# Kernel tuning notes

Hardware: AMD Instinct MI355X
Metric: run time of the kernel (lower is better)

Reference implementation:

```python
import jax, jax.numpy as jnp
import numpy as np

B, C, D, H, W = 1, 128, 8, 32, 32
NH, HD = 8, 16            # num_heads, head_dim = C // NH
PD, PH, PW = 2, 4, 4      # local patch dims
RD, RH, RW = 2, 2, 2      # global K/V reduction ratios
MLPH = 4 * C              # mlp_ratio = 4
EPS = 1e-5
SCALE = HD ** -0.5


def setup_inputs() -> dict:
    key = jax.random.key(0)
    ks = iter(jax.random.split(key, 16))
    def w(shape, scale=0.02):
        return jax.random.normal(next(ks), shape, jnp.float32) * scale
    inp = {"x": jax.random.normal(next(ks), (B, C, D, H, W), jnp.float32)}
    for p in ("l", "g"):  # local branch / global branch transformer blocks
        inp[f"{p}_n1_g"] = jnp.ones((C,), jnp.float32)
        inp[f"{p}_n1_b"] = jnp.zeros((C,), jnp.float32)
        inp[f"{p}_qkv_w"] = w((3 * C, C))            # Linear(dim, 3*dim, bias=False)
        inp[f"{p}_proj_w"] = w((C, C))
        inp[f"{p}_proj_b"] = jnp.zeros((C,), jnp.float32)
        inp[f"{p}_n2_g"] = jnp.ones((C,), jnp.float32)
        inp[f"{p}_n2_b"] = jnp.zeros((C,), jnp.float32)
        inp[f"{p}_fc1_w"] = w((MLPH, C))
        inp[f"{p}_fc1_b"] = jnp.zeros((MLPH,), jnp.float32)
        inp[f"{p}_fc2_w"] = w((C, MLPH))
        inp[f"{p}_fc2_b"] = jnp.zeros((C,), jnp.float32)
    inp["g_ke_w"] = w((C, C, RD, RH, RW))  # Conv3d(dim, dim, k=stride=(2,2,2), bias=False)
    inp["g_ve_w"] = w((C, C, RD, RH, RW))
    inp["g_nk_g"] = jnp.ones((HD,), jnp.float32)
    inp["g_nk_b"] = jnp.zeros((HD,), jnp.float32)
    inp["g_nv_g"] = jnp.ones((HD,), jnp.float32)
    inp["g_nv_b"] = jnp.zeros((HD,), jnp.float32)
    return inp


def _ln(t, g, b):
    m = t.mean(-1, keepdims=True)
    v = jnp.square(t - m).mean(-1, keepdims=True)
    return (t - m) * jax.lax.rsqrt(v + EPS) * g + b


def _mlp(t, w1, b1, w2, b2):
    return jax.nn.gelu(t @ w1.T + b1, approximate=False) @ w2.T + b2


def _forward(x, l_n1_g, l_n1_b, l_qkv_w, l_proj_w, l_proj_b, l_n2_g, l_n2_b,
             l_fc1_w, l_fc1_b, l_fc2_w, l_fc2_b,
             g_n1_g, g_n1_b, g_qkv_w, g_ke_w, g_ve_w, g_nk_g, g_nk_b,
             g_nv_g, g_nv_b, g_proj_w, g_proj_b, g_n2_g, g_n2_b,
             g_fc1_w, g_fc1_b, g_fc2_w, g_fc2_b):
    nd, nh, nw = D // PD, H // PH, W // PW
    R, Npl = nd * nh * nw, PD * PH * PW
    N = D * H * W

    # ---------------- Local branch ----------------
    # (B,C,D,H,W) -> (B, R, Npl, C) patch tokens
    loc = x.reshape(B, C, nd, PD, nh, PH, nw, PW)
    loc = loc.transpose(0, 2, 4, 6, 3, 5, 7, 1).reshape(B, R, Npl, C)
    y = _ln(loc, l_n1_g, l_n1_b)
    qkv = (y @ l_qkv_w.T).reshape(B, R, Npl, 3, NH, HD).transpose(3, 0, 1, 4, 2, 5)
    q, k, v = qkv[0], qkv[1], qkv[2]  # (B,R,NH,Npl,HD)
    attn = jax.nn.softmax(jnp.einsum('brhnd,brhmd->brhnm', q, k) * SCALE, axis=-1)
    o = jnp.einsum('brhnm,brhmd->brhnd', attn, v)
    # faithful to torch: (attn@v).transpose(-1,-2).reshape(B,R,Npl,C)
    o = jnp.swapaxes(o, -1, -2).reshape(B, R, Npl, C)
    loc = loc + (o @ l_proj_w.T + l_proj_b)
    loc = loc + _mlp(_ln(loc, l_n2_g, l_n2_b), l_fc1_w, l_fc1_b, l_fc2_w, l_fc2_b)
    # back to (B,C,D,H,W)
    loc_y = loc.reshape(B, nd, nh, nw, PD, PH, PW, C)
    loc_y = loc_y.transpose(0, 7, 1, 4, 2, 5, 3, 6).reshape(B, C, D, H, W)

    # ---------------- Global branch ----------------
    g = x.reshape(B, C, N).transpose(0, 2, 1)  # (B,N,C)
    y = _ln(g, g_n1_g, g_n1_b)
    qkv = y @ g_qkv_w.T  # (B,N,3C)
    q, k, v = jnp.split(qkv, 3, axis=-1)
    qh = q.reshape(B, N, NH, HD).transpose(0, 2, 1, 3)  # (B,NH,N,HD)
    dn = ('NCDHW', 'OIDHW', 'NCDHW')
    def _reduce(t, wc):
        tm = t.transpose(0, 2, 1).reshape(B, C, D, H, W)
        tr = jax.lax.conv_general_dilated(tm, wc, (RD, RH, RW), 'VALID',
                                          dimension_numbers=dn)
        nr = tr.shape[2] * tr.shape[3] * tr.shape[4]
        return tr.reshape(B, C, nr).transpose(0, 2, 1).reshape(B, nr, NH, HD).transpose(0, 2, 1, 3)
    kr = _ln(_reduce(k, g_ke_w), g_nk_g, g_nk_b)  # (B,NH,Nr,HD)
    vr = _ln(_reduce(v, g_ve_w), g_nv_g, g_nv_b)
    attn = jax.nn.softmax(jnp.einsum('bhnd,bhmd->bhnm', qh, kr) * SCALE, axis=-1)
    o = jnp.einsum('bhnm,bhmd->bhnd', attn, vr)
    o = o.transpose(0, 2, 1, 3).reshape(B, N, C)
    g = g + (o @ g_proj_w.T + g_proj_b)
    g = g + _mlp(_ln(g, g_n2_g, g_n2_b), g_fc1_w, g_fc1_b, g_fc2_w, g_fc2_b)
    glo_y = g.transpose(0, 2, 1).reshape(B, C, D, H, W)

    # ---------------- Gate ----------------
    return x * jax.nn.sigmoid(loc_y + glo_y)


def reference(x, l_n1_g, l_n1_b, l_qkv_w, l_proj_w, l_proj_b, l_n2_g, l_n2_b,
              l_fc1_w, l_fc1_b, l_fc2_w, l_fc2_b,
              g_n1_g, g_n1_b, g_qkv_w, g_ke_w, g_ve_w, g_nk_g, g_nk_b,
              g_nv_g, g_nv_b, g_proj_w, g_proj_b, g_n2_g, g_n2_b,
              g_fc1_w, g_fc1_b, g_fc2_w, g_fc2_b):
    return _forward(x, l_n1_g, l_n1_b, l_qkv_w, l_proj_w, l_proj_b, l_n2_g, l_n2_b,
                    l_fc1_w, l_fc1_b, l_fc2_w, l_fc2_b,
                    g_n1_g, g_n1_b, g_qkv_w, g_ke_w, g_ve_w, g_nk_g, g_nk_b,
                    g_nv_g, g_nv_b, g_proj_w, g_proj_b, g_n2_g, g_n2_b,
                    g_fc1_w, g_fc1_b, g_fc2_w, g_fc2_b)
```

## Files before the change

### kernel.cpp

```cpp
#include <hip/hip_runtime.h>
#include <math.h>

#define N_TOK 8192
#define C_DIM 128
#define NHD   8
#define HDIM  16
#define NR    1024
#define EPSV  1e-5f
#define QK_SCALE 0.25f
#define QK_L2E  0.36067376f

typedef __attribute__((ext_vector_type(8))) short short8;
typedef __attribute__((ext_vector_type(4))) float f32x4;

__device__ __forceinline__ float gelu_f(float v) {
    float u = 0.7978845608f * (v + 0.044715f * v * v * v);
    float e = exp2f(2.885390082f * u);
    return v * (e / (e + 1.0f));
}
__device__ __forceinline__ float uaf(unsigned int u) {
    union { unsigned int u; float f; } x; x.u = u; return x.f;
}
__device__ __forceinline__ short f2b(float v) {
    union { float f; unsigned int u; } x; x.f = v;
    unsigned int r = x.u + 0x7fffu + ((x.u >> 16) & 1u);
    return (short)(r >> 16);
}
__device__ __forceinline__ unsigned int pk2(float a, float b) {
    return (unsigned int)(unsigned short)f2b(a) | ((unsigned int)(unsigned short)f2b(b) << 16);
}
__device__ __forceinline__ void ld16bf(const short* p, float* d) {
    uint4 a = *(const uint4*)p;
    uint4 b = *(const uint4*)(p + 8);
    d[0]  = uaf(a.x << 16); d[1]  = uaf(a.x & 0xffff0000u);
    d[2]  = uaf(a.y << 16); d[3]  = uaf(a.y & 0xffff0000u);
    d[4]  = uaf(a.z << 16); d[5]  = uaf(a.z & 0xffff0000u);
    d[6]  = uaf(a.w << 16); d[7]  = uaf(a.w & 0xffff0000u);
    d[8]  = uaf(b.x << 16); d[9]  = uaf(b.x & 0xffff0000u);
    d[10] = uaf(b.y << 16); d[11] = uaf(b.y & 0xffff0000u);
    d[12] = uaf(b.z << 16); d[13] = uaf(b.z & 0xffff0000u);
    d[14] = uaf(b.w << 16); d[15] = uaf(b.w & 0xffff0000u);
}

__device__ __forceinline__ void gload16(const void* g, void* l) {
    __builtin_amdgcn_global_load_lds(
        (const __attribute__((address_space(1))) unsigned int*)g,
        (__attribute__((address_space(3))) unsigned int*)l, 16, 0, 0);
}

struct CvtDesc { const float* src; short* dst; int n; int pad; };
struct CvtArgs { CvtDesc d[10]; };

__global__ __launch_bounds__(256) void prep_k(const float* __restrict__ x,
                                              const float* __restrict__ g1, const float* __restrict__ b1,
                                              const float* __restrict__ g2, const float* __restrict__ b2,
                                              float* __restrict__ xt,
                                              short* __restrict__ o1, short* __restrict__ o2,
                                              CvtArgs ca) {
    __shared__ float tile[32][132];
    int t = threadIdx.x;
    if (blockIdx.x >= 256) {
        int bid = blockIdx.x - 256;
#pragma unroll 1
        for (int d = 0; d < 10; ++d) {
            CvtDesc dd = ca.d[d];
            if (dd.pad) {
                for (int i = bid * 256 + t; i < dd.n; i += 40 * 256) {
                    int co = i >> 10, qq = i & 1023;
                    dd.dst[co * 1024 + ((qq & 7) << 7) + (qq >> 3)] = f2b(dd.src[i]);
                }
            } else {
                for (int i = bid * 256 + t; i < dd.n; i += 40 * 256)
                    dd.dst[i] = f2b(dd.src[i]);
            }
        }
        return;
    }
    int n0 = blockIdx.x * 32;
#pragma unroll
    for (int k = 0; k < 16; ++k) {
        int f = t + k * 256;
        int n = f & 31, c = f >> 5;
        tile[n][c] = x[(size_t)c * N_TOK + n0 + n];
    }
    __syncthreads();
    int tk = t >> 3, cb = (t & 7) * 16;
    float v[16];
    float s = 0.f, sq = 0.f;
#pragma unroll
    for (int i = 0; i < 16; ++i) {
        v[i] = tile[tk][cb + i];
        s += v[i]; sq += v[i] * v[i];
    }
    s += __shfl_xor(s, 1);  s += __shfl_xor(s, 2);  s += __shfl_xor(s, 4);
    sq += __shfl_xor(sq, 1); sq += __shfl_xor(sq, 2); sq += __shfl_xor(sq, 4);
    float m = s * (1.0f / 128.0f);
    float var = sq * (1.0f / 128.0f) - m * m;
    float rs = rsqrtf(var + EPSV);
    int tok = n0 + tk;
    float* xp = xt + (size_t)tok * C_DIM + cb;
    *(float4*)(xp)      = make_float4(v[0], v[1], v[2], v[3]);
    *(float4*)(xp + 4)  = make_float4(v[4], v[5], v[6], v[7]);
    *(float4*)(xp + 8)  = make_float4(v[8], v[9], v[10], v[11]);
    *(float4*)(xp + 12) = make_float4(v[12], v[13], v[14], v[15]);
    float hA[16], hB[16];
#pragma unroll
    for (int i = 0; i < 16; ++i) {
        float hn = (v[i] - m) * rs;
        hA[i] = hn * g1[cb + i] + b1[cb + i];
        hB[i] = hn * g2[cb + i] + b2[cb + i];
    }
    uint4 ua0 = {pk2(hA[0], hA[1]), pk2(hA[2], hA[3]), pk2(hA[4], hA[5]), pk2(hA[6], hA[7])};
    uint4 ua1 = {pk2(hA[8], hA[9]), pk2(hA[10], hA[11]), pk2(hA[12], hA[13]), pk2(hA[14], hA[15])};
    uint4 ub0 = {pk2(hB[0], hB[1]), pk2(hB[2], hB[3]), pk2(hB[4], hB[5]), pk2(hB[6], hB[7])};
    uint4 ub1 = {pk2(hB[8], hB[9]), pk2(hB[10], hB[11]), pk2(hB[12], hB[13]), pk2(hB[14], hB[15])};
    *(uint4*)(o1 + (size_t)tok * C_DIM + cb)     = ua0;
    *(uint4*)(o1 + (size_t)tok * C_DIM + cb + 8) = ua1;
    *(uint4*)(o2 + (size_t)tok * C_DIM + cb)     = ub0;
    *(uint4*)(o2 + (size_t)tok * C_DIM + cb + 8) = ub1;
}

__global__ __launch_bounds__(256) void ln2_pair_k(const float* __restrict__ in0,
                                                  const float* __restrict__ g0, const float* __restrict__ b0,
                                                  short* __restrict__ o0,
                                                  const float* __restrict__ in1,
                                                  const float* __restrict__ g1, const float* __restrict__ b1,
                                                  short* __restrict__ o1) {
    int blk = blockIdx.x;
    bool sel = blk >= 2048;
    blk &= 2047;
    const float* in = sel ? in1 : in0;
    const float* g  = sel ? g1 : g0;
    const float* b  = sel ? b1 : b0;
    short* o        = sel ? o1 : o0;
    int lane = threadIdx.x & 63;
    int n = blk * 4 + (threadIdx.x >> 6);
    float v0 = in[(size_t)n * C_DIM + lane];
    float v1 = in[(size_t)n * C_DIM + 64 + lane];
    float s = v0 + v1, sq = v0 * v0 + v1 * v1;
#pragma unroll
    for (int off = 32; off >= 1; off >>= 1) {
        s += __shfl_xor(s, off);
        sq += __shfl_xor(sq, off);
    }
    float m = s * (1.0f / 128.0f);
    float var = sq * (1.0f / 128.0f) - m * m;
    float rs = rsqrtf(var + EPSV);
    o[(size_t)n * C_DIM + lane]      = f2b((v0 - m) * rs * g[lane] + b[lane]);
    o[(size_t)n * C_DIM + 64 + lane] = f2b((v1 - m) * rs * g[lane + 64] + b[lane + 64]);
}

struct MArgs {
    const short* A[2]; const short* W[2];
    const float* bias[2]; const float* res[2];
    void* out[2];
};
template <int EPI>
__global__ __launch_bounds__(256) void mgemm_k(MArgs ga, int M, int N, int K) {
    int zi = blockIdx.z;
    const short* A = ga.A[zi];
    const short* W = ga.W[zi];
    __shared__ short As[2][128 * 64];
    __shared__ short Bs[2][128 * 64];
    int t = threadIdx.x;
    int w = t >> 6, l = t & 63;
    int m0 = blockIdx.x * 128, n0 = blockIdx.y * 128;
    int wm = (w >> 1) * 64, wn = (w & 1) * 64;

    f32x4 acc[4][4];
#pragma unroll
    for (int a = 0; a < 4; ++a)
#pragma unroll
        for (int b = 0; b < 4; ++b) acc[a][b] = f32x4{0.f, 0.f, 0.f, 0.f};

    auto STAGE = [&](int buf, int k0) {
#pragma unroll
        for (int c = 0; c < 4; ++c) {
            int g0 = c * 256 + w * 64;
            int g  = g0 + l;
            int row = g >> 3, ss = g & 7;
            int slot = ss ^ (row & 7);
            gload16(A + (size_t)(m0 + row) * K + k0 + slot * 8, &As[buf][g0 * 8]);
            gload16(W + (size_t)(n0 + row) * K + k0 + slot * 8, &Bs[buf][g0 * 8]);
        }
    };

    int NT = K >> 6;
    STAGE(0, 0);
    int cur = 0;
    for (int it = 0; it < NT; ++it) {
        if (it + 1 < NT) {
            STAGE(cur ^ 1, (it + 1) << 6);
            asm volatile("s_waitcnt vmcnt(8)" ::: "memory");
        } else {
            asm volatile("s_waitcnt vmcnt(0)" ::: "memory");
        }
        __builtin_amdgcn_s_barrier();
#pragma unroll
        for (int kk = 0; kk < 2; ++kk) {
            short8 af[4], bf[4];
            int sl = kk * 4 + (l >> 4);
#pragma unroll
            for (int mf = 0; mf < 4; ++mf) {
                int row = wm + mf * 16 + (l & 15);
                af[mf] = *(const short8*)(&As[cur][row * 64 + (sl ^ (row & 7)) * 8]);
            }
#pragma unroll
            for (int nf = 0; nf < 4; ++nf) {
                int row = wn + nf * 16 + (l & 15);
                bf[nf] = *(const short8*)(&Bs[cur][row * 64 + (sl ^ (row & 7)) * 8]);
            }
#pragma unroll
            for (int mf = 0; mf < 4; ++mf)
#pragma unroll
                for (int nf = 0; nf < 4; ++nf)
                    acc[mf][nf] = __builtin_amdgcn_mfma_f32_16x16x32_bf16(
                        af[mf], bf[nf], acc[mf][nf], 0, 0, 0);
        }
        asm volatile("s_waitcnt lgkmcnt(0)" ::: "memory");
        __builtin_amdgcn_sched_barrier(0);
        __builtin_amdgcn_s_barrier();
        cur ^= 1;
    }

#pragma unroll
    for (int mf = 0; mf < 4; ++mf) {
#pragma unroll
        for (int nf = 0; nf < 4; ++nf) {
            int col = n0 + wn + nf * 16 + (l & 15);
#pragma unroll
            for (int j = 0; j < 4; ++j) {
                int row = m0 + wm + mf * 16 + (l >> 4) * 4 + j;
                float v = acc[mf][nf][j];
                if (EPI == 0) {
                    ((short*)ga.out[zi])[(size_t)row * N + col] = f2b(v);
                } else if (EPI == 1) {
                    v += ga.bias[zi][col] + ga.res[zi][(size_t)row * N + col];
                    ((float*)ga.out[zi])[(size_t)row * N + col] = v;
                } else if (EPI == 2) {
                    v = gelu_f(v + ga.bias[zi][col]);
                    ((short*)ga.out[zi])[(size_t)row * N + col] = f2b(v);
                }
            }
        }
    }
}

struct CLArgs {
    const short* qkv_g; const short* wk; const short* wv;
    float* kpart; float* vpart;
    const short* qkv_l; short* ob;
};
__global__ __launch_bounds__(256) void convlat_k(CLArgs ga) {
    __shared__ char smem[65536];
    int t = threadIdx.x;
    if (blockIdx.x < 128) {
        int bid = blockIdx.x;
        int m0 = (bid & 7) * 128;
        int zi = bid >> 6;
        int slice = (bid >> 3) & 7;
        const short* Abase = ga.qkv_g + (zi ? 256 : 128);
        const short* W = zi ? ga.wv : ga.wk;
        float* outp = zi ? ga.vpart : ga.kpart;
        short (*As)[8192] = (short(*)[8192])smem;
        short (*Bs)[8192] = (short(*)[8192])(smem + 32768);
        int w = t >> 6, l = t & 63;
        int wm = (w >> 1) * 64, wn = (w & 1) * 64;
        int kbeg = slice * 128;
        int od = slice >> 2, oh = (slice >> 1) & 1, ow = slice & 1;

        f32x4 acc[4][4];
#pragma unroll
        for (int a = 0; a < 4; ++a)
#pragma unroll
            for (int b = 0; b < 4; ++b) acc[a][b] = f32x4{0.f, 0.f, 0.f, 0.f};

        auto STAGE = [&](int buf, int k0) {
#pragma unroll
            for (int c = 0; c < 4; ++c) {
                int g0 = c * 256 + w * 64;
                int g  = g0 + l;
                int row = g >> 3, ss = g & 7;
                int slot = ss ^ (row & 7);
                int nr = m0 + row;
                int n = (2 * (nr >> 8) + od) * 1024 + (2 * ((nr >> 4) & 15) + oh) * 32
                        + 2 * (nr & 15) + ow;
                gload16(Abase + (size_t)n * 384 + (k0 & 127) + slot * 8, &As[buf][g0 * 8]);
                gload16(W + (size_t)row * 1024 + k0 + slot * 8, &Bs[buf][g0 * 8]);
            }
        };

        STAGE(0, kbeg);
        int cur = 0;
        for (int it = 0; it < 2; ++it) {
            if (it == 0) {
                STAGE(1, kbeg + 64);
                asm volatile("s_waitcnt vmcnt(8)" ::: "memory");
            } else {
                asm volatile("s_waitcnt vmcnt(0)" ::: "memory");
            }
            __builtin_amdgcn_s_barrier();
#pragma unroll
            for (int kk = 0; kk < 2; ++kk) {
                short8 af[4], bf[4];
                int sl = kk * 4 + (l >> 4);
#pragma unroll
                for (int mf = 0; mf < 4; ++mf) {
                    int row = wm + mf * 16 + (l & 15);
                    af[mf] = *(const short8*)(&As[cur][row * 64 + (sl ^ (row & 7)) * 8]);
                }
#pragma unroll
                for (int nf = 0; nf < 4; ++nf) {
                    int row = wn + nf * 16 + (l & 15);
                    bf[nf] = *(const short8*)(&Bs[cur][row * 64 + (sl ^ (row & 7)) * 8]);
                }
#pragma unroll
                for (int mf = 0; mf < 4; ++mf)
#pragma unroll
                    for (int nf = 0; nf < 4; ++nf)
                        acc[mf][nf] = __builtin_amdgcn_mfma_f32_16x16x32_bf16(
                            af[mf], bf[nf], acc[mf][nf], 0, 0, 0);
            }
            asm volatile("s_waitcnt lgkmcnt(0)" ::: "memory");
            __builtin_amdgcn_sched_barrier(0);
            __builtin_amdgcn_s_barrier();
            cur ^= 1;
        }
#pragma unroll
        for (int mf = 0; mf < 4; ++mf)
#pragma unroll
            for (int nf = 0; nf < 4; ++nf) {
                int col = wn + nf * 16 + (l & 15);
#pragma unroll
                for (int j = 0; j < 4; ++j) {
                    int row = m0 + wm + mf * 16 + (l >> 4) * 4 + j;
                    outp[(size_t)slice * (NR * C_DIM) + (size_t)row * C_DIM + col] =
                        acc[mf][nf][j];
                }
            }
        return;
    }
    float (*ks)[32][HDIM] = (float(*)[32][HDIM])smem;
    float (*vs)[32][HDIM] = (float(*)[32][HDIM])(smem + 16384);
    int m = t & 31, h = t >> 5, r = blockIdx.x - 128;
    int zd = r >> 6, zh = (r >> 3) & 7, zw = r & 7;
    int pd = m >> 4, ph = (m >> 2) & 3, pw = m & 3;
    int n = (zd * 2 + pd) * 1024 + (zh * 4 + ph) * 32 + (zw * 4 + pw);
    const short* base = ga.qkv_l + (size_t)n * 384 + h * HDIM;
    float q[16], kt[16], vt[16];
    ld16bf(base, q);
    ld16bf(base + 128, kt);
    ld16bf(base + 256, vt);
#pragma unroll
    for (int d = 0; d < 16; ++d) { ks[h][m][d] = kt[d]; vs[h][m][d] = vt[d]; }
    __syncthreads();
    float s[32];
#pragma unroll
    for (int j = 0; j < 32; ++j) {
        float d = 0.f;
#pragma unroll
        for (int dd = 0; dd < 16; ++dd) d += q[dd] * ks[h][j][dd];
        s[j] = __expf(d * QK_SCALE);
    }
    float sum = 0.f;
#pragma unroll
    for (int j = 0; j < 32; ++j) sum += s[j];
    float inv = 1.0f / sum;
    float oo[16] = {};
#pragma unroll
    for (int j = 0; j < 32; ++j) {
        float p = s[j] * inv;
#pragma unroll
        for (int dd = 0; dd < 16; ++dd) oo[dd] += p * vs[h][j][dd];
    }
#pragma unroll
    for (int dd = 0; dd < 16; ++dd) {
        int n2 = h * 4 + (dd >> 2);
        int c2 = (dd & 3) * 32 + m;
        int pd2 = n2 >> 4, ph2 = (n2 >> 2) & 3, pw2 = n2 & 3;
        int nn = (zd * 2 + pd2) * 1024 + (zh * 4 + ph2) * 32 + (zw * 4 + pw2);
        ga.ob[(size_t)nn * C_DIM + c2] = f2b(oo[dd]);
    }
}

__global__ __launch_bounds__(256) void ln_head_sum_k(const float* __restrict__ kpart,
                                                     const float* __restrict__ vpart,
                                                     const float* __restrict__ gk, const float* __restrict__ bk,
                                                     const float* __restrict__ gv, const float* __restrict__ bv,
                                                     short* __restrict__ kout, short* __restrict__ vout) {
    __shared__ float vlds[8][16][33];
    int t = threadIdx.x;
    bool sel = blockIdx.x >= 32;
    int b = sel ? (blockIdx.x - 32) : blockIdx.x;
    int id2 = b * 256 + t;
    const float* part = sel ? vpart : kpart;
    const float* g    = sel ? gv : gk;
    const float* bb   = sel ? bv : bk;
    int nr = id2 >> 3, h = id2 & 7;
    size_t base = (size_t)nr * C_DIM + h * HDIM;
    float v[16] = {};
#pragma unroll
    for (int p = 0; p < 8; ++p) {
        const float* pp = part + (size_t)p * (NR * C_DIM) + base;
#pragma unroll
        for (int d4 = 0; d4 < 4; ++d4) {
            float4 tv = *(const float4*)(pp + d4 * 4);
            v[d4 * 4 + 0] += tv.x; v[d4 * 4 + 1] += tv.y;
            v[d4 * 4 + 2] += tv.z; v[d4 * 4 + 3] += tv.w;
        }
    }
    float s = 0.f;
#pragma unroll
    for (int i = 0; i < 16; ++i) s += v[i];
    float m = s * (1.0f / 16.0f);
    float sq = 0.f;
#pragma unroll
    for (int i = 0; i < 16; ++i) { float d = v[i] - m; sq += d * d; }
    float rs = rsqrtf(sq * (1.0f / 16.0f) + EPSV);
    if (!sel) {
        short* op = kout + (size_t)h * (NR * HDIM) + (size_t)nr * HDIM;
#pragma unroll
        for (int i = 0; i < 16; ++i)
            op[i] = f2b(((v[i] - m) * rs * g[i] + bb[i]) * QK_L2E);
        return;
    }
    int nr_l = t >> 3;
#pragma unroll
    for (int i = 0; i < 16; ++i)
        vlds[h][i][nr_l] = (v[i] - m) * rs * g[i] + bb[i];
    __syncthreads();
    int row = t >> 1, half = t & 1;
    int h2 = row >> 4, i2 = row & 15;
    const float* src = &vlds[h2][i2][half * 16];
    uint4 u0 = {pk2(src[0], src[1]), pk2(src[2], src[3]), pk2(src[4], src[5]), pk2(src[6], src[7])};
    uint4 u1 = {pk2(src[8], src[9]), pk2(src[10], src[11]), pk2(src[12], src[13]), pk2(src[14], src[15])};
    short* dst = vout + (size_t)h2 * (HDIM * NR) + (size_t)i2 * NR + b * 32 + half * 16;
    *(uint4*)(dst)     = u0;
    *(uint4*)(dst + 8) = u1;
}

__global__ __launch_bounds__(512) void gattn_k(const short* __restrict__ qkv,
                                               const short* __restrict__ kb,
                                               const short* __restrict__ vt,
                                               short* __restrict__ ob) {
    __shared__ short plds[8][2048];
    __shared__ float comb[4][64][5];
    int t = threadIdx.x;
    int w = t >> 6, l = t & 63;
    int h = blockIdx.y;
    int lr = l & 15, lq = l >> 4;
    int qw = w & 3, kw = w >> 2;
    int q0 = blockIdx.x * 64 + qw * 16;

    short8 qf = short8{0, 0, 0, 0, 0, 0, 0, 0};
    if (lq < 2)
        qf = *(const short8*)(qkv + (size_t)(q0 + lr) * 384 + h * HDIM + lq * 8);

    const short* kh = kb + (size_t)h * (NR * HDIM);
    const short* vh = vt + (size_t)h * (HDIM * NR);
    short* pw = &plds[w][0];

    const f32x4 zz = {0.f, 0.f, 0.f, 0.f};
    f32x4 oacc = {0.f, 0.f, 0.f, 0.f};
    float rs = 0.f;

    for (int c = 0; c < 4; ++c) {
        int kbase = kw * 512 + c * 128;
        f32x4 s[8];
#pragma unroll
        for (int nf = 0; nf < 8; ++nf) {
            short8 kf = short8{0, 0, 0, 0, 0, 0, 0, 0};
            if (lq < 2)
                kf = *(const short8*)(kh + (size_t)(kbase + nf * 16 + lr) * HDIM + lq * 8);
            s[nf] = __builtin_amdgcn_mfma_f32_16x16x32_bf16(kf, qf, zz, 0, 0, 0);
        }
#pragma unroll
        for (int nf = 0; nf < 8; ++nf) {
            float p0 = exp2f(s[nf][0]);
            float p1 = exp2f(s[nf][1]);
            float p2 = exp2f(s[nf][2]);
            float p3 = exp2f(s[nf][3]);
            rs += (p0 + p1) + (p2 + p3);
            unsigned int u01, u23;
            asm("v_cvt_pk_bf16_f32 %0, %1, %2" : "=v"(u01) : "v"(p0), "v"(p1));
            asm("v_cvt_pk_bf16_f32 %0, %1, %2" : "=v"(u23) : "v"(p2), "v"(p3));
            int k0 = nf * 16 + lq * 4;
            int sw = (lr & 7) << 3;
            *(unsigned int*)&pw[lr * 128 + (k0 ^ sw)]       = u01;
            *(unsigned int*)&pw[lr * 128 + ((k0 + 2) ^ sw)] = u23;
        }
#pragma unroll
        for (int ks = 0; ks < 4; ++ks) {
            short8 pf = *(const short8*)&pw[(lr * 128 + ks * 32 + lq * 8) ^ ((lr & 7) << 3)];
            short8 vf = *(const short8*)(vh + (size_t)lr * NR + kbase + ks * 32 + lq * 8);
            oacc = __builtin_amdgcn_mfma_f32_16x16x32_bf16(pf, vf, oacc, 0, 0, 0);
        }
    }
    rs += __shfl_xor(rs, 16);
    rs += __shfl_xor(rs, 32);
    if (w >= 4) {
        comb[w - 4][l][0] = oacc[0];
        comb[w - 4][l][1] = oacc[1];
        comb[w - 4][l][2] = oacc[2];
        comb[w - 4][l][3] = oacc[3];
        comb[w - 4][l][4] = rs;
    }
    __syncthreads();
    if (w < 4) {
        oacc[0] += comb[w][l][0];
        oacc[1] += comb[w][l][1];
        oacc[2] += comb[w][l][2];
        oacc[3] += comb[w][l][3];
        rs += comb[w][l][4];
        float r0 = __shfl(rs, lq * 4 + 0);
        float r1 = __shfl(rs, lq * 4 + 1);
        float r2 = __shfl(rs, lq * 4 + 2);
        float r3 = __shfl(rs, lq * 4 + 3);
        size_t base_o = (size_t)(q0 + lq * 4) * C_DIM + h * HDIM + lr;
        ob[base_o]             = f2b(oacc[0] / r0);
        ob[base_o + C_DIM]     = f2b(oacc[1] / r1);
        ob[base_o + 2 * C_DIM] = f2b(oacc[2] / r2);
        ob[base_o + 3 * C_DIM] = f2b(oacc[3] / r3);
    }
}

__global__ __launch_bounds__(256) void gate_k(const float* __restrict__ x,
                                              const float* __restrict__ lf, const float* __restrict__ gf,
                                              float* __restrict__ out) {
    __shared__ float tile[32][33];
    int n0 = blockIdx.x * 32, c0 = blockIdx.y * 32;
    int tx = threadIdx.x, ty = threadIdx.y;
#pragma unroll
    for (int k = 0; k < 4; ++k) {
        int n = n0 + ty + k * 8, c = c0 + tx;
        tile[ty + k * 8][tx] = lf[(size_t)n * C_DIM + c] + gf[(size_t)n * C_DIM + c];
    }
    __syncthreads();
#pragma unroll
    for (int k = 0; k < 4; ++k) {
        int c = c0 + ty + k * 8, n = n0 + tx;
        float z = tile[tx][ty + k * 8];
        float sg = 1.0f / (1.0f + __expf(-z));
        out[(size_t)c * N_TOK + n] = x[(size_t)c * N_TOK + n] * sg;
    }
}

extern "C" void kernel_launch(void* const* d_in, const int* in_sizes, int n_in,
                              void* d_out, int out_size, void* d_ws, size_t ws_size,
                              hipStream_t stream) {
    const float* x        = (const float*)d_in[0];
    const float* l_n1_g   = (const float*)d_in[1];
    const float* l_n1_b   = (const float*)d_in[2];
    const float* l_qkv_w  = (const float*)d_in[3];
    const float* l_proj_w = (const float*)d_in[4];
    const float* l_proj_b = (const float*)d_in[5];
    const float* l_n2_g   = (const float*)d_in[6];
    const float* l_n2_b   = (const float*)d_in[7];
    const float* l_fc1_w  = (const float*)d_in[8];
    const float* l_fc1_b  = (const float*)d_in[9];
    const float* l_fc2_w  = (const float*)d_in[10];
    const float* l_fc2_b  = (const float*)d_in[11];
    const float* g_n1_g   = (const float*)d_in[12];
    const float* g_n1_b   = (const float*)d_in[13];
    const float* g_qkv_w  = (const float*)d_in[14];
    const float* g_proj_w = (const float*)d_in[15];
    const float* g_proj_b = (const float*)d_in[16];
    const float* g_n2_g   = (const float*)d_in[17];
    const float* g_n2_b   = (const float*)d_in[18];
    const float* g_fc1_w  = (const float*)d_in[19];
    const float* g_fc1_b  = (const float*)d_in[20];
    const float* g_fc2_w  = (const float*)d_in[21];
    const float* g_fc2_b  = (const float*)d_in[22];
    const float* g_ke_w   = (const float*)d_in[23];
    const float* g_ve_w   = (const float*)d_in[24];
    const float* g_nk_g   = (const float*)d_in[25];
    const float* g_nk_b   = (const float*)d_in[26];
    const float* g_nv_g   = (const float*)d_in[27];
    const float* g_nv_b   = (const float*)d_in[28];
    float* out = (float*)d_out;

    char* base = (char*)d_ws;
    float* xt     = (float*)(base);
    float* t1_l   = (float*)(base + (4ull  << 20));
    float* t1_g   = (float*)(base + (8ull  << 20));
    short* yA16   = (short*)(base + (12ull << 20));
    short* yG16   = (short*)(base + (14ull << 20));
    short* t2_l   = yA16;
    short* t2_g   = yG16;
    float* locfin = (float*)(base + (12ull << 20));
    short* obuf_l = (short*)(base + (16ull << 20));
    short* obuf_g = (short*)(base + (18ull << 20));
    float* glofin = (float*)(base + (16ull << 20));
    short* qkv_l  = (short*)(base + (20ull << 20));
    short* qkv_g  = (short*)(base + (26ull << 20));
    short* h1_l   = (short*)(base + (32ull << 20));
    float* kpart  = (float*)(base + (32ull << 20));
    float* vpart  = (float*)(base + (36ull << 20));
    short* h1_g   = (short*)(base + (40ull << 20));
    short* kb16   = (short*)(base + (48ull << 20));
    short* vt16   = (short*)(base + (48ull << 20) + (512ull << 10));
    short* wts    = (short*)(base + (49ull << 20));

    const int L_QKV = 0,      L_PROJ = 49152, L_FC1 = 65536,  L_FC2 = 131072;
    const int G_QKV = 196608, G_PROJ = 245760, G_FC1 = 262144, G_FC2 = 327680;
    const int G_KE  = 393216, G_VE   = 524288;

    CvtArgs ca;
    ca.d[0] = {l_qkv_w,  wts + L_QKV,  49152, 0};
    ca.d[1] = {l_proj_w, wts + L_PROJ, 16384, 0};
    ca.d[2] = {l_fc1_w,  wts + L_FC1,  65536, 0};
    ca.d[3] = {l_fc2_w,  wts + L_FC2,  65536, 0};
    ca.d[4] = {g_qkv_w,  wts + G_QKV,  49152, 0};
    ca.d[5] = {g_proj_w, wts + G_PROJ, 16384, 0};
    ca.d[6] = {g_fc1_w,  wts + G_FC1,  65536, 0};
    ca.d[7] = {g_fc2_w,  wts + G_FC2,  65536, 0};
    ca.d[8] = {g_ke_w,   wts + G_KE,  131072, 1};
    ca.d[9] = {g_ve_w,   wts + G_VE,  131072, 1};

    prep_k<<<296, 256, 0, stream>>>(x, l_n1_g, l_n1_b, g_n1_g, g_n1_b, xt, yA16, yG16, ca);

    MArgs a_qkv = {{yA16, yG16}, {wts + L_QKV, wts + G_QKV}, {nullptr, nullptr}, {nullptr, nullptr}, {qkv_l, qkv_g}};
    mgemm_k<0><<<dim3(64, 3, 2), 256, 0, stream>>>(a_qkv, N_TOK, 384, 128);

    CLArgs cla = {qkv_g, wts + G_KE, wts + G_VE, kpart, vpart, qkv_l, obuf_l};
    convlat_k<<<384, 256, 0, stream>>>(cla);

    ln_head_sum_k<<<64, 256, 0, stream>>>(kpart, vpart, g_nk_g, g_nk_b, g_nv_g, g_nv_b, kb16, vt16);

    gattn_k<<<dim3(128, 8), 512, 0, stream>>>(qkv_g, kb16, vt16, obuf_g);

    MArgs a_pj = {{obuf_l, obuf_g}, {wts + L_PROJ, wts + G_PROJ}, {l_proj_b, g_proj_b}, {xt, xt}, {t1_l, t1_g}};
    mgemm_k<1><<<dim3(64, 1, 2), 256, 0, stream>>>(a_pj, N_TOK, 128, 128);

    ln2_pair_k<<<4096, 256, 0, stream>>>(t1_l, l_n2_g, l_n2_b, t2_l, t1_g, g_n2_g, g_n2_b, t2_g);

    MArgs a_f1 = {{t2_l, t2_g}, {wts + L_FC1, wts + G_FC1}, {l_fc1_b, g_fc1_b}, {nullptr, nullptr}, {h1_l, h1_g}};
    mgemm_k<2><<<dim3(64, 4, 2), 256, 0, stream>>>(a_f1, N_TOK, 512, 128);

    MArgs a_f2 = {{h1_l, h1_g}, {wts + L_FC2, wts + G_FC2}, {l_fc2_b, g_fc2_b}, {t1_l, t1_g}, {locfin, glofin}};
    mgemm_k<1><<<dim3(64, 1, 2), 256, 0, stream>>>(a_f2, N_TOK, 128, 512);

    gate_k<<<dim3(256, 4), dim3(32, 8), 0, stream>>>(x, locfin, glofin, out);
}
```

Measured before the change: 137.9 us.

## Fuse LN2 into proj epilogue, gate into fc2, and re-stage branch GEMMs

The proj GEMM epilogue now computes LayerNorm2 through an LDS tile, and the global fc2 epilogue applies the sigmoid gate with a transpose. This removes the separate ln2 and gate kernels. The local and global branch GEMMs are re-staged into mixed-role launches so that independent work from the two branches shares a kernel (local proj with K/V LN, global proj with local fc1, global fc1 with local fc2). This cuts launch count and intermediate traffic, but the global fc2 stage runs only 64 blocks and each launch mixes heterogeneous work.

```diff
diff --git a/kernel.cpp b/kernel.cpp
--- a/kernel.cpp
+++ b/kernel.cpp
@@ -41,7 +41,6 @@
     d[12] = uaf(b.z << 16); d[13] = uaf(b.z & 0xffff0000u);
     d[14] = uaf(b.w << 16); d[15] = uaf(b.w & 0xffff0000u);
 }
-
 __device__ __forceinline__ void gload16(const void* g, void* l) {
     __builtin_amdgcn_global_load_lds(
         (const __attribute__((address_space(1))) unsigned int*)g,
@@ -50,6 +49,206 @@
 
 struct CvtDesc { const float* src; short* dst; int n; int pad; };
 struct CvtArgs { CvtDesc d[10]; };
+
+__device__ __forceinline__ void mm128(const short* __restrict__ A, const short* __restrict__ W,
+                                      int K, int m0, int n0, int t, char* smem,
+                                      f32x4 acc[4][4]) {
+    short* As0 = (short*)smem;
+    short* Bs0 = (short*)(smem + 32768);
+    int w = t >> 6, l = t & 63;
+    auto STAGE = [&](int buf, int k0) {
+        short* As = As0 + buf * 8192;
+        short* Bs = Bs0 + buf * 8192;
+#pragma unroll
+        for (int c = 0; c < 4; ++c) {
+            int g0 = c * 256 + w * 64;
+            int g  = g0 + l;
+            int row = g >> 3, ss = g & 7;
+            int slot = ss ^ (row & 7);
+            gload16(A + (size_t)(m0 + row) * K + k0 + slot * 8, As + g0 * 8);
+            gload16(W + (size_t)(n0 + row) * K + k0 + slot * 8, Bs + g0 * 8);
+        }
+    };
+    int wm = (w >> 1) * 64, wn = (w & 1) * 64;
+    int NT = K >> 6;
+    STAGE(0, 0);
+    int cur = 0;
+    for (int it = 0; it < NT; ++it) {
+        if (it + 1 < NT) {
+            STAGE(cur ^ 1, (it + 1) << 6);
+            asm volatile("s_waitcnt vmcnt(8)" ::: "memory");
+        } else {
+            asm volatile("s_waitcnt vmcnt(0)" ::: "memory");
+        }
+        __builtin_amdgcn_s_barrier();
+        short* As = As0 + cur * 8192;
+        short* Bs = Bs0 + cur * 8192;
+#pragma unroll
+        for (int kk = 0; kk < 2; ++kk) {
+            short8 af[4], bf[4];
+            int sl = kk * 4 + (l >> 4);
+#pragma unroll
+            for (int mf = 0; mf < 4; ++mf) {
+                int row = wm + mf * 16 + (l & 15);
+                af[mf] = *(const short8*)(&As[row * 64 + (sl ^ (row & 7)) * 8]);
+            }
+#pragma unroll
+            for (int nf = 0; nf < 4; ++nf) {
+                int row = wn + nf * 16 + (l & 15);
+                bf[nf] = *(const short8*)(&Bs[row * 64 + (sl ^ (row & 7)) * 8]);
+            }
+#pragma unroll
+            for (int mf = 0; mf < 4; ++mf)
+#pragma unroll
+                for (int nf = 0; nf < 4; ++nf)
+                    acc[mf][nf] = __builtin_amdgcn_mfma_f32_16x16x32_bf16(
+                        af[mf], bf[nf], acc[mf][nf], 0, 0, 0);
+        }
+        asm volatile("s_waitcnt lgkmcnt(0)" ::: "memory");
+        __builtin_amdgcn_sched_barrier(0);
+        __builtin_amdgcn_s_barrier();
+        cur ^= 1;
+    }
+}
+
+template <int GELU>
+__device__ __forceinline__ void epi_bf16(f32x4 acc[4][4], const float* bias, short* out,
+                                         int m0, int n0, int N, int t) {
+    int w = t >> 6, l = t & 63;
+    int wm = (w >> 1) * 64, wn = (w & 1) * 64;
+#pragma unroll
+    for (int mf = 0; mf < 4; ++mf)
+#pragma unroll
+        for (int nf = 0; nf < 4; ++nf) {
+            int col = n0 + wn + nf * 16 + (l & 15);
+#pragma unroll
+            for (int j = 0; j < 4; ++j) {
+                int row = m0 + wm + mf * 16 + (l >> 4) * 4 + j;
+                float v = acc[mf][nf][j];
+                if (GELU) v = gelu_f(v + bias[col]);
+                out[(size_t)row * N + col] = f2b(v);
+            }
+        }
+}
+
+__device__ __forceinline__ void epi_res(f32x4 acc[4][4], const float* bias, const float* res,
+                                        float* out, int m0, int N, int t) {
+    int w = t >> 6, l = t & 63;
+    int wm = (w >> 1) * 64, wn = (w & 1) * 64;
+#pragma unroll
+    for (int mf = 0; mf < 4; ++mf)
+#pragma unroll
+        for (int nf = 0; nf < 4; ++nf) {
+            int col = wn + nf * 16 + (l & 15);
+#pragma unroll
+            for (int j = 0; j < 4; ++j) {
+                int row = m0 + wm + mf * 16 + (l >> 4) * 4 + j;
+                float v = acc[mf][nf][j] + bias[col] + res[(size_t)row * N + col];
+                out[(size_t)row * N + col] = v;
+            }
+        }
+}
+
+__device__ __forceinline__ void proj_ln_epi(f32x4 acc[4][4], const float* bias,
+        const float* res, float* t1, short* t2, const float* g, const float* b,
+        int m0, int t, char* smem) {
+    int w = t >> 6, l = t & 63;
+    int wm = (w >> 1) * 64, wn = (w & 1) * 64;
+    float* zl = (float*)smem;
+#pragma unroll
+    for (int half = 0; half < 2; ++half) {
+        if ((wm >> 6) == half) {
+#pragma unroll
+            for (int mf = 0; mf < 4; ++mf)
+#pragma unroll
+                for (int nf = 0; nf < 4; ++nf) {
+                    int col = wn + nf * 16 + (l & 15);
+#pragma unroll
+                    for (int j = 0; j < 4; ++j) {
+                        int row = wm + mf * 16 + (l >> 4) * 4 + j;
+                        float v = acc[mf][nf][j] + bias[col] + res[(size_t)(m0 + row) * C_DIM + col];
+                        t1[(size_t)(m0 + row) * C_DIM + col] = v;
+                        zl[(row & 63) * 129 + col] = v;
+                    }
+                }
+        }
+        __syncthreads();
+        {
+            int r = t >> 2, seg = (t & 3) * 32;
+            const float* zr = zl + r * 129 + seg;
+            float vv[32];
+            float s = 0.f, sq = 0.f;
+#pragma unroll
+            for (int i = 0; i < 32; ++i) { vv[i] = zr[i]; s += vv[i]; sq += vv[i] * vv[i]; }
+            s += __shfl_xor(s, 1);  s += __shfl_xor(s, 2);
+            sq += __shfl_xor(sq, 1); sq += __shfl_xor(sq, 2);
+            float m = s * (1.0f / 128.0f);
+            float var = sq * (1.0f / 128.0f) - m * m;
+            float rsq = rsqrtf(var + EPSV);
+            int tok = m0 + half * 64 + r;
+            short* op = t2 + (size_t)tok * C_DIM + seg;
+            float o[32];
+#pragma unroll
+            for (int i = 0; i < 32; ++i) o[i] = (vv[i] - m) * rsq * g[seg + i] + b[seg + i];
+#pragma unroll
+            for (int q = 0; q < 4; ++q) {
+                uint4 u;
+                u.x = pk2(o[q * 8 + 0], o[q * 8 + 1]);
+                u.y = pk2(o[q * 8 + 2], o[q * 8 + 3]);
+                u.z = pk2(o[q * 8 + 4], o[q * 8 + 5]);
+                u.w = pk2(o[q * 8 + 6], o[q * 8 + 7]);
+                *(uint4*)(op + q * 8) = u;
+            }
+        }
+        __syncthreads();
+    }
+}
+
+__device__ __forceinline__ void gate_epi(f32x4 acc[4][4], const float* bias,
+        const float* res, const float* locf, const float* xin, float* outp,
+        int m0, int t, char* smem) {
+    int w = t >> 6, l = t & 63;
+    int wm = (w >> 1) * 64, wn = (w & 1) * 64;
+    float* zl = (float*)smem;
+#pragma unroll
+    for (int half = 0; half < 2; ++half) {
+        if ((wm >> 6) == half) {
+#pragma unroll
+            for (int mf = 0; mf < 4; ++mf)
+#pragma unroll
+                for (int nf = 0; nf < 4; ++nf) {
+                    int col = wn + nf * 16 + (l & 15);
+#pragma unroll
+                    for (int j = 0; j < 4; ++j) {
+                        int row = wm + mf * 16 + (l >> 4) * 4 + j;
+                        size_t idx = (size_t)(m0 + row) * C_DIM + col;
+                        float v = acc[mf][nf][j] + bias[col] + res[idx];
+                        zl[(row & 63) * 129 + col] = locf[idx] + v;
+                    }
+                }
+        }
+        __syncthreads();
+        {
+            int c = t >> 1, mseg = (t & 1) * 32;
+            size_t gb = (size_t)c * N_TOK + m0 + half * 64 + mseg;
+#pragma unroll
+            for (int mm = 0; mm < 32; mm += 4) {
+                float4 xv = *(const float4*)(xin + gb + mm);
+                float z0 = zl[(mseg + mm + 0) * 129 + c];
+                float z1 = zl[(mseg + mm + 1) * 129 + c];
+                float z2 = zl[(mseg + mm + 2) * 129 + c];
+                float z3 = zl[(mseg + mm + 3) * 129 + c];
+                float4 ov;
+                ov.x = xv.x / (1.0f + __expf(-z0));
+                ov.y = xv.y / (1.0f + __expf(-z1));
+                ov.z = xv.z / (1.0f + __expf(-z2));
+                ov.w = xv.w / (1.0f + __expf(-z3));
+                *(float4*)(outp + gb + mm) = ov;
+            }
+        }
+        __syncthreads();
+    }
+}
 
 __global__ __launch_bounds__(256) void prep_k(const float* __restrict__ x,
                                               const float* __restrict__ g1, const float* __restrict__ b1,
@@ -120,130 +319,20 @@
     *(uint4*)(o2 + (size_t)tok * C_DIM + cb + 8) = ub1;
 }
 
-__global__ __launch_bounds__(256) void ln2_pair_k(const float* __restrict__ in0,
-                                                  const float* __restrict__ g0, const float* __restrict__ b0,
-                                                  short* __restrict__ o0,
-                                                  const float* __restrict__ in1,
-                                                  const float* __restrict__ g1, const float* __restrict__ b1,
-                                                  short* __restrict__ o1) {
-    int blk = blockIdx.x;
-    bool sel = blk >= 2048;
-    blk &= 2047;
-    const float* in = sel ? in1 : in0;
-    const float* g  = sel ? g1 : g0;
-    const float* b  = sel ? b1 : b0;
-    short* o        = sel ? o1 : o0;
-    int lane = threadIdx.x & 63;
-    int n = blk * 4 + (threadIdx.x >> 6);
-    float v0 = in[(size_t)n * C_DIM + lane];
-    float v1 = in[(size_t)n * C_DIM + 64 + lane];
-    float s = v0 + v1, sq = v0 * v0 + v1 * v1;
-#pragma unroll
-    for (int off = 32; off >= 1; off >>= 1) {
-        s += __shfl_xor(s, off);
-        sq += __shfl_xor(sq, off);
-    }
-    float m = s * (1.0f / 128.0f);
-    float var = sq * (1.0f / 128.0f) - m * m;
-    float rs = rsqrtf(var + EPSV);
-    o[(size_t)n * C_DIM + lane]      = f2b((v0 - m) * rs * g[lane] + b[lane]);
-    o[(size_t)n * C_DIM + 64 + lane] = f2b((v1 - m) * rs * g[lane + 64] + b[lane + 64]);
-}
-
 struct MArgs {
     const short* A[2]; const short* W[2];
-    const float* bias[2]; const float* res[2];
     void* out[2];
 };
-template <int EPI>
-__global__ __launch_bounds__(256) void mgemm_k(MArgs ga, int M, int N, int K) {
+__global__ __launch_bounds__(256) void qkv_k(MArgs ga, int M, int N, int K) {
+    __shared__ char smem[65536];
     int zi = blockIdx.z;
-    const short* A = ga.A[zi];
-    const short* W = ga.W[zi];
-    __shared__ short As[2][128 * 64];
-    __shared__ short Bs[2][128 * 64];
-    int t = threadIdx.x;
-    int w = t >> 6, l = t & 63;
-    int m0 = blockIdx.x * 128, n0 = blockIdx.y * 128;
-    int wm = (w >> 1) * 64, wn = (w & 1) * 64;
-
     f32x4 acc[4][4];
 #pragma unroll
     for (int a = 0; a < 4; ++a)
 #pragma unroll
         for (int b = 0; b < 4; ++b) acc[a][b] = f32x4{0.f, 0.f, 0.f, 0.f};
-
-    auto STAGE = [&](int buf, int k0) {
-#pragma unroll
-        for (int c = 0; c < 4; ++c) {
-            int g0 = c * 256 + w * 64;
-            int g  = g0 + l;
-            int row = g >> 3, ss = g & 7;
-            int slot = ss ^ (row & 7);
-            gload16(A + (size_t)(m0 + row) * K + k0 + slot * 8, &As[buf][g0 * 8]);
-            gload16(W + (size_t)(n0 + row) * K + k0 + slot * 8, &Bs[buf][g0 * 8]);
-        }
-    };
-
-    int NT = K >> 6;
-    STAGE(0, 0);
-    int cur = 0;
-    for (int it = 0; it < NT; ++it) {
-        if (it + 1 < NT) {
-            STAGE(cur ^ 1, (it + 1) << 6);
-            asm volatile("s_waitcnt vmcnt(8)" ::: "memory");
-        } else {
-            asm volatile("s_waitcnt vmcnt(0)" ::: "memory");
-        }
-        __builtin_amdgcn_s_barrier();
-#pragma unroll
-        for (int kk = 0; kk < 2; ++kk) {
-            short8 af[4], bf[4];
-            int sl = kk * 4 + (l >> 4);
-#pragma unroll
-            for (int mf = 0; mf < 4; ++mf) {
-                int row = wm + mf * 16 + (l & 15);
-                af[mf] = *(const short8*)(&As[cur][row * 64 + (sl ^ (row & 7)) * 8]);
-            }
-#pragma unroll
-            for (int nf = 0; nf < 4; ++nf) {
-                int row = wn + nf * 16 + (l & 15);
-                bf[nf] = *(const short8*)(&Bs[cur][row * 64 + (sl ^ (row & 7)) * 8]);
-            }
-#pragma unroll
-            for (int mf = 0; mf < 4; ++mf)
-#pragma unroll
-                for (int nf = 0; nf < 4; ++nf)
-                    acc[mf][nf] = __builtin_amdgcn_mfma_f32_16x16x32_bf16(
-                        af[mf], bf[nf], acc[mf][nf], 0, 0, 0);
-        }
-        asm volatile("s_waitcnt lgkmcnt(0)" ::: "memory");
-        __builtin_amdgcn_sched_barrier(0);
-        __builtin_amdgcn_s_barrier();
-        cur ^= 1;
-    }
-
-#pragma unroll
-    for (int mf = 0; mf < 4; ++mf) {
-#pragma unroll
-        for (int nf = 0; nf < 4; ++nf) {
-            int col = n0 + wn + nf * 16 + (l & 15);
-#pragma unroll
-            for (int j = 0; j < 4; ++j) {
-                int row = m0 + wm + mf * 16 + (l >> 4) * 4 + j;
-                float v = acc[mf][nf][j];
-                if (EPI == 0) {
-                    ((short*)ga.out[zi])[(size_t)row * N + col] = f2b(v);
-                } else if (EPI == 1) {
-                    v += ga.bias[zi][col] + ga.res[zi][(size_t)row * N + col];
-                    ((float*)ga.out[zi])[(size_t)row * N + col] = v;
-                } else if (EPI == 2) {
-                    v = gelu_f(v + ga.bias[zi][col]);
-                    ((short*)ga.out[zi])[(size_t)row * N + col] = f2b(v);
-                }
-            }
-        }
-    }
+    mm128(ga.A[zi], ga.W[zi], K, blockIdx.x * 128, blockIdx.y * 128, threadIdx.x, smem, acc);
+    epi_bf16<0>(acc, nullptr, (short*)ga.out[zi], blockIdx.x * 128, blockIdx.y * 128, N, threadIdx.x);
 }
 
 struct CLArgs {
@@ -383,19 +472,34 @@
     }
 }
 
-__global__ __launch_bounds__(256) void ln_head_sum_k(const float* __restrict__ kpart,
-                                                     const float* __restrict__ vpart,
-                                                     const float* __restrict__ gk, const float* __restrict__ bk,
-                                                     const float* __restrict__ gv, const float* __restrict__ bv,
-                                                     short* __restrict__ kout, short* __restrict__ vout) {
-    __shared__ float vlds[8][16][33];
+struct S4Args {
+    const short* obuf_l; const short* wproj; const float* pbias; const float* xt;
+    float* t1; short* t2; const float* lng; const float* lnb;
+    const float* kpart; const float* vpart;
+    const float* gk; const float* bk; const float* gv; const float* bv;
+    short* kout; short* vout;
+};
+__global__ __launch_bounds__(256) void s4_k(S4Args a) {
+    __shared__ char smem[65536];
     int t = threadIdx.x;
-    bool sel = blockIdx.x >= 32;
-    int b = sel ? (blockIdx.x - 32) : blockIdx.x;
-    int id2 = b * 256 + t;
-    const float* part = sel ? vpart : kpart;
-    const float* g    = sel ? gv : gk;
-    const float* bb   = sel ? bv : bk;
+    if (blockIdx.x < 64) {
+        f32x4 acc[4][4];
+#pragma unroll
+        for (int i = 0; i < 4; ++i)
+#pragma unroll
+            for (int j = 0; j < 4; ++j) acc[i][j] = f32x4{0.f, 0.f, 0.f, 0.f};
+        mm128(a.obuf_l, a.wproj, 128, blockIdx.x * 128, 0, t, smem, acc);
+        proj_ln_epi(acc, a.pbias, a.xt, a.t1, a.t2, a.lng, a.lnb, blockIdx.x * 128, t, smem);
+        return;
+    }
+    float (*vlds)[16][33] = (float(*)[16][33])smem;
+    int b = blockIdx.x - 64;
+    bool sel = b >= 32;
+    int bb2 = sel ? (b - 32) : b;
+    int id2 = bb2 * 256 + t;
+    const float* part = sel ? a.vpart : a.kpart;
+    const float* g    = sel ? a.gv : a.gk;
+    const float* bbv  = sel ? a.bv : a.bk;
     int nr = id2 >> 3, h = id2 & 7;
     size_t base = (size_t)nr * C_DIM + h * HDIM;
     float v[16] = {};
@@ -418,23 +522,23 @@
     for (int i = 0; i < 16; ++i) { float d = v[i] - m; sq += d * d; }
     float rs = rsqrtf(sq * (1.0f / 16.0f) + EPSV);
     if (!sel) {
-        short* op = kout + (size_t)h * (NR * HDIM) + (size_t)nr * HDIM;
+        short* op = a.kout + (size_t)h * (NR * HDIM) + (size_t)nr * HDIM;
 #pragma unroll
         for (int i = 0; i < 16; ++i)
-            op[i] = f2b(((v[i] - m) * rs * g[i] + bb[i]) * QK_L2E);
+            op[i] = f2b(((v[i] - m) * rs * g[i] + bbv[i]) * QK_L2E);
         return;
     }
     int nr_l = t >> 3;
 #pragma unroll
     for (int i = 0; i < 16; ++i)
-        vlds[h][i][nr_l] = (v[i] - m) * rs * g[i] + bb[i];
+        vlds[h][i][nr_l] = (v[i] - m) * rs * g[i] + bbv[i];
     __syncthreads();
     int row = t >> 1, half = t & 1;
     int h2 = row >> 4, i2 = row & 15;
     const float* src = &vlds[h2][i2][half * 16];
     uint4 u0 = {pk2(src[0], src[1]), pk2(src[2], src[3]), pk2(src[4], src[5]), pk2(src[6], src[7])};
     uint4 u1 = {pk2(src[8], src[9]), pk2(src[10], src[11]), pk2(src[12], src[13]), pk2(src[14], src[15])};
-    short* dst = vout + (size_t)h2 * (HDIM * NR) + (size_t)i2 * NR + b * 32 + half * 16;
+    short* dst = a.vout + (size_t)h2 * (HDIM * NR) + (size_t)i2 * NR + bb2 * 32 + half * 16;
     *(uint4*)(dst)     = u0;
     *(uint4*)(dst + 8) = u1;
 }
@@ -524,25 +628,68 @@
     }
 }
 
-__global__ __launch_bounds__(256) void gate_k(const float* __restrict__ x,
-                                              const float* __restrict__ lf, const float* __restrict__ gf,
-                                              float* __restrict__ out) {
-    __shared__ float tile[32][33];
-    int n0 = blockIdx.x * 32, c0 = blockIdx.y * 32;
-    int tx = threadIdx.x, ty = threadIdx.y;
-#pragma unroll
-    for (int k = 0; k < 4; ++k) {
-        int n = n0 + ty + k * 8, c = c0 + tx;
-        tile[ty + k * 8][tx] = lf[(size_t)n * C_DIM + c] + gf[(size_t)n * C_DIM + c];
-    }
-    __syncthreads();
-#pragma unroll
-    for (int k = 0; k < 4; ++k) {
-        int c = c0 + ty + k * 8, n = n0 + tx;
-        float z = tile[tx][ty + k * 8];
-        float sg = 1.0f / (1.0f + __expf(-z));
-        out[(size_t)c * N_TOK + n] = x[(size_t)c * N_TOK + n] * sg;
-    }
+struct S6Args {
+    const short* obuf_g; const short* wproj; const float* pbias; const float* xt;
+    float* t1; short* t2; const float* lng; const float* lnb;
+    const short* t2l; const short* wfc1; const float* f1bias; short* h1;
+};
+__global__ __launch_bounds__(256) void s6_k(S6Args a) {
+    __shared__ char smem[65536];
+    int t = threadIdx.x;
+    f32x4 acc[4][4];
+#pragma unroll
+    for (int i = 0; i < 4; ++i)
+#pragma unroll
+        for (int j = 0; j < 4; ++j) acc[i][j] = f32x4{0.f, 0.f, 0.f, 0.f};
+    if (blockIdx.x < 64) {
+        mm128(a.obuf_g, a.wproj, 128, blockIdx.x * 128, 0, t, smem, acc);
+        proj_ln_epi(acc, a.pbias, a.xt, a.t1, a.t2, a.lng, a.lnb, blockIdx.x * 128, t, smem);
+    } else {
+        int bid = blockIdx.x - 64;
+        int m0 = (bid & 63) * 128, n0 = (bid >> 6) * 128;
+        mm128(a.t2l, a.wfc1, 128, m0, n0, t, smem, acc);
+        epi_bf16<1>(acc, a.f1bias, a.h1, m0, n0, 512, t);
+    }
+}
+
+struct S7Args {
+    const short* t2g; const short* wfc1; const float* f1bias; short* h1g;
+    const short* h1l; const short* wfc2; const float* f2bias; const float* t1l; float* locfin;
+};
+__global__ __launch_bounds__(256) void s7_k(S7Args a) {
+    __shared__ char smem[65536];
+    int t = threadIdx.x;
+    f32x4 acc[4][4];
+#pragma unroll
+    for (int i = 0; i < 4; ++i)
+#pragma unroll
+        for (int j = 0; j < 4; ++j) acc[i][j] = f32x4{0.f, 0.f, 0.f, 0.f};
+    if (blockIdx.x < 256) {
+        int m0 = (blockIdx.x & 63) * 128, n0 = (blockIdx.x >> 6) * 128;
+        mm128(a.t2g, a.wfc1, 128, m0, n0, t, smem, acc);
+        epi_bf16<1>(acc, a.f1bias, a.h1g, m0, n0, 512, t);
+    } else {
+        int m0 = (blockIdx.x - 256) * 128;
+        mm128(a.h1l, a.wfc2, 512, m0, 0, t, smem, acc);
+        epi_res(acc, a.f2bias, a.t1l, a.locfin, m0, 128, t);
+    }
+}
+
+struct S8Args {
+    const short* h1g; const short* wfc2; const float* f2bias; const float* t1g;
+    const float* locfin; const float* xin; float* outp;
+};
+__global__ __launch_bounds__(256) void s8_k(S8Args a) {
+    __shared__ char smem[65536];
+    int t = threadIdx.x;
+    f32x4 acc[4][4];
+#pragma unroll
+    for (int i = 0; i < 4; ++i)
+#pragma unroll
+        for (int j = 0; j < 4; ++j) acc[i][j] = f32x4{0.f, 0.f, 0.f, 0.f};
+    int m0 = blockIdx.x * 128;
+    mm128(a.h1g, a.wfc2, 512, m0, 0, t, smem, acc);
+    gate_epi(acc, a.f2bias, a.t1g, a.locfin, a.xin, a.outp, m0, t, smem);
 }
 
 extern "C" void kernel_launch(void* const* d_in, const int* in_sizes, int n_in,
@@ -587,15 +734,14 @@
     short* yG16   = (short*)(base + (14ull << 20));
     short* t2_l   = yA16;
     short* t2_g   = yG16;
-    float* locfin = (float*)(base + (12ull << 20));
     short* obuf_l = (short*)(base + (16ull << 20));
     short* obuf_g = (short*)(base + (18ull << 20));
-    float* glofin = (float*)(base + (16ull << 20));
+    float* locfin = (float*)(base + (16ull << 20));
     short* qkv_l  = (short*)(base + (20ull << 20));
     short* qkv_g  = (short*)(base + (26ull << 20));
-    short* h1_l   = (short*)(base + (32ull << 20));
     float* kpart  = (float*)(base + (32ull << 20));
     float* vpart  = (float*)(base + (36ull << 20));
+    short* h1_l   = (short*)(base + (32ull << 20));
     short* h1_g   = (short*)(base + (40ull << 20));
     short* kb16   = (short*)(base + (48ull << 20));
     short* vt16   = (short*)(base + (48ull << 20) + (512ull << 10));
@@ -619,26 +765,26 @@
 
     prep_k<<<296, 256, 0, stream>>>(x, l_n1_g, l_n1_b, g_n1_g, g_n1_b, xt, yA16, yG16, ca);
 
-    MArgs a_qkv = {{yA16, yG16}, {wts + L_QKV, wts + G_QKV}, {nullptr, nullptr}, {nullptr, nullptr}, {qkv_l, qkv_g}};
-    mgemm_k<0><<<dim3(64, 3, 2), 256, 0, stream>>>(a_qkv, N_TOK, 384, 128);
+    MArgs a_qkv = {{yA16, yG16}, {wts + L_QKV, wts + G_QKV}, {qkv_l, qkv_g}};
+    qkv_k<<<dim3(64, 3, 2), 256, 0, stream>>>(a_qkv, N_TOK, 384, 128);
 
     CLArgs cla = {qkv_g, wts + G_KE, wts + G_VE, kpart, vpart, qkv_l, obuf_l};
     convlat_k<<<384, 256, 0, stream>>>(cla);
 
-    ln_head_sum_k<<<64, 256, 0, stream>>>(kpart, vpart, g_nk_g, g_nk_b, g_nv_g, g_nv_b, kb16, vt16);
+    S4Args a4 = {obuf_l, wts + L_PROJ, l_proj_b, xt, t1_l, t2_l, l_n2_g, l_n2_b,
+                 kpart, vpart, g_nk_g, g_nk_b, g_nv_g, g_nv_b, kb16, vt16};
+    s4_k<<<128, 256, 0, stream>>>(a4);
 
     gattn_k<<<dim3(128, 8), 512, 0, stream>>>(qkv_g, kb16, vt16, obuf_g);
 
-    MArgs a_pj = {{obuf_l, obuf_g}, {wts + L_PROJ, wts + G_PROJ}, {l_proj_b, g_proj_b}, {xt, xt}, {t1_l, t1_g}};
-    mgemm_k<1><<<dim3(64, 1, 2), 256, 0, stream>>>(a_pj, N_TOK, 128, 128);
-
-    ln2_pair_k<<<4096, 256, 0, stream>>>(t1_l, l_n2_g, l_n2_b, t2_l, t1_g, g_n2_g, g_n2_b, t2_g);
-
-    MArgs a_f1 = {{t2_l, t2_g}, {wts + L_FC1, wts + G_FC1}, {l_fc1_b, g_fc1_b}, {nullptr, nullptr}, {h1_l, h1_g}};
-    mgemm_k<2><<<dim3(64, 4, 2), 256, 0, stream>>>(a_f1, N_TOK, 512, 128);
-
-    MArgs a_f2 = {{h1_l, h1_g}, {wts + L_FC2, wts + G_FC2}, {l_fc2_b, g_fc2_b}, {t1_l, t1_g}, {locfin, glofin}};
-    mgemm_k<1><<<dim3(64, 1, 2), 256, 0, stream>>>(a_f2, N_TOK, 128, 512);
-
-    gate_k<<<dim3(256, 4), dim3(32, 8), 0, stream>>>(x, locfin, glofin, out);
-}
+    S6Args a6 = {obuf_g, wts + G_PROJ, g_proj_b, xt, t1_g, t2_g, g_n2_g, g_n2_b,
+                 t2_l, wts + L_FC1, l_fc1_b, h1_l};
+    s6_k<<<320, 256, 0, stream>>>(a6);
+
+    S7Args a7 = {t2_g, wts + G_FC1, g_fc1_b, h1_g,
+                 h1_l, wts + L_FC2, l_fc2_b, t1_l, locfin};
+    s7_k<<<320, 256, 0, stream>>>(a7);
+
+    S8Args a8 = {h1_g, wts + G_FC2, g_fc2_b, t1_g, locfin, x, out};
+    s8_k<<<64, 256, 0, stream>>>(a8);
+}
```

After: 174.8 us. 1.27x slower.
